# Optimization experiments

Measured on AMD Instinct MI355X. Metric: run time of the kernel, lower is better.

Reference implementation:

```python
import jax, jax.numpy as jnp
import numpy as np

CHUNK = 64   # hyperparams['chunk_size']
HEADS = 16   # hyperparams['n_heads']


def _chunk_mask(T, cs):
    # Faithful reproduction of the original (buggy) chunked mask:
    # for chunk pair with q-chunk start i and k-chunk start j, masking is applied
    # only when i >= j, with triu(diagonal = j - i + 1). Algebraically this masks
    # position (q, k) iff q_block_start >= k_block_start and
    #   (k - q) - 2*(k_block_start - q_block_start) >= 1.
    idx = jnp.arange(T)
    blk = (idx // cs) * cs  # chunk start of each position
    qb = blk[:, None]
    kb = blk[None, :]
    masked = (qb >= kb) & ((idx[None, :] - idx[:, None] - 2 * (kb - qb)) >= 1)
    return masked  # [T, T], True = set score to -inf


def setup_inputs() -> dict:
    key = jax.random.key(0)
    ks = jax.random.split(key, 6)
    B, T, C = 2, 2048, 1024
    w = 0.02  # init scale so softmax is not saturated
    return {
        "x": jax.random.normal(ks[0], (B, T, C), jnp.float32),
        "Wq": jax.random.normal(ks[1], (C, C), jnp.float32) * w,
        "bq": jnp.zeros((C,), jnp.float32),
        "Wk": jax.random.normal(ks[2], (C, C), jnp.float32) * w,
        "bk": jnp.zeros((C,), jnp.float32),
        "Wv": jax.random.normal(ks[3], (C, C), jnp.float32) * w,
        "bv": jnp.zeros((C,), jnp.float32),
        "Wo": jax.random.normal(ks[4], (C, C), jnp.float32) * w,
        "bo": jnp.zeros((C,), jnp.float32),
        "attn_scale": jnp.full((1,), 1.0 / np.sqrt(C // HEADS), jnp.float32),
    }


def reference(x, Wq, bq, Wk, bk, Wv, bv, Wo, bo, attn_scale):
    B, T, C = x.shape
    H = HEADS
    D = C // H
    # torch nn.Linear: y = x @ W.T + b
    q = (x @ Wq.T + bq).reshape(B, T, H, D)
    k = (x @ Wk.T + bk).reshape(B, T, H, D)
    v = (x @ Wv.T + bv).reshape(B, T, H, D)
    scores = jnp.einsum("bqhd,bkhd->bhqk", q, k) * attn_scale[0]
    mask = _chunk_mask(T, CHUNK)  # [T, T]
    scores = jnp.where(mask[None, None], -jnp.inf, scores)
    attn = jax.nn.softmax(scores, axis=-1)  # [B, H, T, T]
    out = jnp.einsum("bhqk,bkhd->bqhd", attn, v).reshape(B, T, C)
    return out @ Wo.T + bo
```

## Files before the change

### kernel.cpp

```cpp
#include <hip/hip_runtime.h>


#define BT 4096
#define TSEQ 2048
#define CDIM 1024

typedef __attribute__((ext_vector_type(8))) short bf16x8;
typedef __attribute__((ext_vector_type(4))) float f32x4;
typedef __attribute__((ext_vector_type(4))) float float4v;
typedef __attribute__((ext_vector_type(4))) unsigned short u16x4;

__device__ __forceinline__ unsigned short f2bf(float x){
  union { float f; unsigned int u; } c; c.f = x;
  unsigned int r = c.u + 0x7FFFu + ((c.u >> 16) & 1u);
  return (unsigned short)(r >> 16);
}
__device__ __forceinline__ float bf2f(unsigned short h){
  union { unsigned int u; float f; } c; c.u = ((unsigned int)h) << 16;
  return c.f;
}
__device__ __forceinline__ f32x4 zero4(){ f32x4 v; v[0]=0.f; v[1]=0.f; v[2]=0.f; v[3]=0.f; return v; }

#define GLDS16(g, l) __builtin_amdgcn_global_load_lds( \
  (const __attribute__((address_space(1))) void*)(g), \
  (__attribute__((address_space(3))) void*)(l), 16, 0, 0)

__global__ __launch_bounds__(256) void k_prep(
    const float* __restrict__ x,
    const float* __restrict__ Wq, const float* __restrict__ Wk,
    const float* __restrict__ Wv, const float* __restrict__ Wo,
    const float* __restrict__ bq, const float* __restrict__ bk, const float* __restrict__ bv,
    unsigned short* __restrict__ xh, unsigned short* __restrict__ wh,
    float* __restrict__ bias_cat){
  const int NX = 1048576;
  const int NTOT = 2097152;
  int i = blockIdx.x * 256 + threadIdx.x;
  if (i < 3072){
    const float* bs[3] = {bq, bk, bv};
    bias_cat[i] = bs[i >> 10][i & 1023];
  }
  int stride = gridDim.x * 256;
  for (; i < NTOT; i += stride){
    float4v v;
    u16x4 h;
    if (i < NX){
      v = ((const float4v*)x)[i];
      #pragma unroll
      for (int j = 0; j < 4; ++j) h[j] = f2bf(v[j]);
      ((u16x4*)xh)[i] = h;
    } else {
      int jj = i - NX;
      const float* srcs[4] = {Wq, Wk, Wv, Wo};
      v = ((const float4v*)srcs[jj >> 18])[jj & 0x3FFFF];
      #pragma unroll
      for (int j = 0; j < 4; ++j) h[j] = f2bf(v[j]);
      ((u16x4*)wh)[jj] = h;
    }
  }
}

template<int BN, int MODE, int SPLITA>
__global__ __launch_bounds__(256) void k_gemm(
    const unsigned short* __restrict__ Ah, const unsigned short* __restrict__ Al,
    const unsigned short* __restrict__ Bh,
    const float* __restrict__ bias,
    unsigned short* __restrict__ oq, unsigned short* __restrict__ okk,
    unsigned short* __restrict__ ov, float* __restrict__ fo)
{
  constexpr int MF = (BN == 128) ? 4 : 2;
  constexpr int NF = 4;
  constexpr int BISS = (BN == 128) ? 2 : 1;
  constexpr int NA = SPLITA ? 2 : 1;
  __shared__ unsigned short As[NA][128*32];
  __shared__ unsigned short Bs[BN*32];

  const int tid  = threadIdx.x;
  const int wid  = tid >> 6;
  const int lane = tid & 63;
  const int l15  = lane & 15;
  const int kg   = lane >> 4;
  const int m0 = blockIdx.y * 128;
  const int n0 = blockIdx.x * BN;
  const int wrb = (BN == 128) ? (wid >> 1) * 64 : wid * 32;
  const int wcb = (BN == 128) ? (wid & 1) * 64 : 0;

  f32x4 acc[MF][NF];
  #pragma unroll
  for (int a = 0; a < MF; ++a)
    #pragma unroll
    for (int b = 0; b < NF; ++b) acc[a][b] = zero4();

  for (int k0 = 0; k0 < 1024; k0 += 32){
    #pragma unroll
    for (int p = 0; p < NA; ++p){
      const unsigned short* Asrc = p ? Al : Ah;
      #pragma unroll
      for (int iss = 0; iss < 2; ++iss){
        int L = iss*2048 + tid*8;
        int row = L >> 5;
        int ck = ((L >> 3) & 3) ^ ((row >> 1) & 3);
        GLDS16(Asrc + (size_t)(m0 + row)*1024 + k0 + ck*8,
               (char*)(&As[p][0]) + iss*4096 + wid*1024);
      }
    }
    #pragma unroll
    for (int iss = 0; iss < BISS; ++iss){
      int L = iss*2048 + tid*8;
      int row = L >> 5;
      int ck = ((L >> 3) & 3) ^ ((row >> 1) & 3);
      GLDS16(Bh + (size_t)(n0 + row)*1024 + k0 + ck*8,
             (char*)(&Bs[0]) + iss*4096 + wid*1024);
    }
    __syncthreads();

    bf16x8 af[MF][NA];
    #pragma unroll
    for (int mf = 0; mf < MF; ++mf){
      int r = wrb + mf*16 + l15;
      int ckpos = kg ^ ((r >> 1) & 3);
      #pragma unroll
      for (int p = 0; p < NA; ++p)
        af[mf][p] = *(const bf16x8*)((const char*)(&As[p][0]) + r*64 + ckpos*16);
    }
    #pragma unroll
    for (int nf = 0; nf < NF; ++nf){
      int r = wcb + nf*16 + l15;
      int ckpos = kg ^ ((r >> 1) & 3);
      bf16x8 bhv = *(const bf16x8*)((const char*)(&Bs[0]) + r*64 + ckpos*16);
      #pragma unroll
      for (int mf = 0; mf < MF; ++mf){
        acc[mf][nf] = __builtin_amdgcn_mfma_f32_16x16x32_bf16(af[mf][0], bhv, acc[mf][nf], 0,0,0);
        if (SPLITA)
          acc[mf][nf] = __builtin_amdgcn_mfma_f32_16x16x32_bf16(af[mf][1], bhv, acc[mf][nf], 0,0,0);
      }
    }
    __syncthreads();
  }

  #pragma unroll
  for (int mf = 0; mf < MF; ++mf){
    #pragma unroll
    for (int nf = 0; nf < NF; ++nf){
      int colg = n0 + wcb + nf*16 + l15;
      float bb = bias[colg];
      #pragma unroll
      for (int j = 0; j < 4; ++j){
        int r = m0 + wrb + mf*16 + kg*4 + j;
        float val = acc[mf][nf][j] + bb;
        if (MODE == 1){
          fo[(size_t)r*1024 + colg] = val;
        } else {
          int bi = r >> 11, tt = r & 2047;
          int mat = colg >> 10, jj = colg & 1023;
          int h = jj >> 6, d = jj & 63;
          size_t bh_ = (size_t)(bi*16 + h);
          unsigned short vv = f2bf(val);
          if (mat == 0)      oq [(bh_*2048 + tt)*64 + d] = vv;
          else if (mat == 1) okk[(bh_*2048 + tt)*64 + d] = vv;
          else               ov [(bh_*64 + d)*2048 + tt] = vv;
        }
      }
    }
  }
}

__global__ __launch_bounds__(256) void k_attn(
    const unsigned short* __restrict__ Qg, const unsigned short* __restrict__ Kg,
    const unsigned short* __restrict__ Vtg, const float* __restrict__ scale_p,
    unsigned short* __restrict__ Ohi, unsigned short* __restrict__ Olo)
{
  __shared__ unsigned short Qs[64*64];
  __shared__ unsigned short Ks[64*64];
  __shared__ unsigned short Vts[64*64];
  __shared__ unsigned short Ps[4][16*64];

  const int tid  = threadIdx.x;
  const int wid  = tid >> 6;
  const int lane = tid & 63;
  const int l15  = lane & 15;
  const int kg   = lane >> 4;
  const int qi = blockIdx.x >> 5;
  const int bh = blockIdx.x & 31;
  const size_t base = (size_t)bh * (2048*64);
  const float scale = scale_p[0];

  #pragma unroll
  for (int iss = 0; iss < 2; ++iss){
    int L = iss*2048 + tid*8;
    int r = L >> 6;
    int ck = ((L >> 3) & 7) ^ (r & 7);
    GLDS16(Qg + base + (size_t)(qi*64 + r)*64 + ck*8, (char*)Qs + iss*4096 + wid*1024);
  }

  f32x4 Ofr[4];
  #pragma unroll
  for (int d = 0; d < 4; ++d) Ofr[d] = zero4();
  float mrow[4] = {-1e30f,-1e30f,-1e30f,-1e30f};
  float lrow[4] = {0.f,0.f,0.f,0.f};

  {
    int kb = qi;
    #pragma unroll
    for (int iss = 0; iss < 2; ++iss){
      int L = iss*2048 + tid*8;
      int r = L >> 6;
      int ck = ((L >> 3) & 7) ^ (r & 7);
      GLDS16(Kg  + base + (size_t)(kb*64 + r)*64 + ck*8, (char*)Ks  + iss*4096 + wid*1024);
      GLDS16(Vtg + base + (size_t)r*2048 + kb*64 + ck*8, (char*)Vts + iss*4096 + wid*1024);
    }
  }
  __syncthreads();

  for (int kb = qi; kb < 32; ++kb){
    f32x4 S[4];
    #pragma unroll
    for (int nf = 0; nf < 4; ++nf) S[nf] = zero4();
    #pragma unroll
    for (int ks = 0; ks < 2; ++ks){
      int rq = wid*16 + l15;
      bf16x8 aq = *(const bf16x8*)((const char*)Qs + rq*128 + (((ks*4 + kg) ^ (rq & 7)) * 16));
      #pragma unroll
      for (int nf = 0; nf < 4; ++nf){
        int rk = nf*16 + l15;
        bf16x8 bk_ = *(const bf16x8*)((const char*)Ks + rk*128 + (((ks*4 + kg) ^ (rk & 7)) * 16));
        S[nf] = __builtin_amdgcn_mfma_f32_16x16x32_bf16(aq, bk_, S[nf], 0,0,0);
      }
    }
    #pragma unroll
    for (int nf = 0; nf < 4; ++nf){
      #pragma unroll
      for (int j = 0; j < 4; ++j){
        float s = S[nf][j] * scale;
        if (kb == qi){
          int ql = wid*16 + kg*4 + j;
          int kk = nf*16 + l15;
          if (kk > ql) s = -1e30f;
        }
        S[nf][j] = s;
      }
    }
    float rm[4], fj[4], rs[4];
    #pragma unroll
    for (int j = 0; j < 4; ++j)
      rm[j] = fmaxf(fmaxf(S[0][j], S[1][j]), fmaxf(S[2][j], S[3][j]));
    #pragma unroll
    for (int d = 1; d < 16; d <<= 1){
      #pragma unroll
      for (int j = 0; j < 4; ++j) rm[j] = fmaxf(rm[j], __shfl_xor(rm[j], d, 64));
    }
    #pragma unroll
    for (int j = 0; j < 4; ++j){
      float mn = fmaxf(mrow[j], rm[j]);
      fj[j] = __expf(mrow[j] - mn);
      mrow[j] = mn;
      rs[j] = 0.f;
    }
    #pragma unroll
    for (int nf = 0; nf < 4; ++nf){
      #pragma unroll
      for (int j = 0; j < 4; ++j){
        float p = __expf(S[nf][j] - mrow[j]);
        S[nf][j] = p;
        rs[j] += p;
      }
    }
    #pragma unroll
    for (int d = 1; d < 16; d <<= 1){
      #pragma unroll
      for (int j = 0; j < 4; ++j) rs[j] += __shfl_xor(rs[j], d, 64);
    }
    #pragma unroll
    for (int j = 0; j < 4; ++j) lrow[j] = lrow[j]*fj[j] + rs[j];
    #pragma unroll
    for (int df = 0; df < 4; ++df){
      #pragma unroll
      for (int j = 0; j < 4; ++j) Ofr[df][j] *= fj[j];
    }
    #pragma unroll
    for (int nf = 0; nf < 4; ++nf){
      #pragma unroll
      for (int j = 0; j < 4; ++j){
        int r = kg*4 + j;
        int c2 = (nf*16 + l15) * 2;
        *(unsigned short*)((char*)(&Ps[wid][0]) + r*128 + (c2 ^ ((r & 7) << 4))) = f2bf(S[nf][j]);
      }
    }
    #pragma unroll
    for (int ks = 0; ks < 2; ++ks){
      bf16x8 pa = *(const bf16x8*)((const char*)(&Ps[wid][0]) + l15*128 + (((ks*4 + kg) ^ (l15 & 7)) * 16));
      #pragma unroll
      for (int df = 0; df < 4; ++df){
        int rv = df*16 + l15;
        bf16x8 vb = *(const bf16x8*)((const char*)Vts + rv*128 + (((ks*4 + kg) ^ (rv & 7)) * 16));
        Ofr[df] = __builtin_amdgcn_mfma_f32_16x16x32_bf16(pa, vb, Ofr[df], 0,0,0);
      }
    }
    __syncthreads();
    if (kb < 31){
      int kb2 = kb + 1;
      #pragma unroll
      for (int iss = 0; iss < 2; ++iss){
        int L = iss*2048 + tid*8;
        int r = L >> 6;
        int ck = ((L >> 3) & 7) ^ (r & 7);
        GLDS16(Kg  + base + (size_t)(kb2*64 + r)*64 + ck*8, (char*)Ks  + iss*4096 + wid*1024);
        GLDS16(Vtg + base + (size_t)r*2048 + kb2*64 + ck*8, (char*)Vts + iss*4096 + wid*1024);
      }
      __syncthreads();
    }
  }

  const int bi = bh >> 4, h = bh & 15;
  #pragma unroll
  for (int df = 0; df < 4; ++df){
    #pragma unroll
    for (int j = 0; j < 4; ++j){
      int tt = qi*64 + wid*16 + kg*4 + j;
      size_t row = (size_t)(bi*2048 + tt);
      int col = h*64 + df*16 + l15;
      float v = Ofr[df][j] / lrow[j];
      unsigned short hv = f2bf(v);
      Ohi[row*1024 + col] = hv;
      Olo[row*1024 + col] = f2bf(v - bf2f(hv));
    }
  }
}

extern "C" void kernel_launch(void* const* d_in, const int* in_sizes, int n_in,
                              void* d_out, int out_size, void* d_ws, size_t ws_size,
                              hipStream_t stream){
  const float* x  = (const float*)d_in[0];
  const float* Wq = (const float*)d_in[1];
  const float* bq = (const float*)d_in[2];
  const float* Wk = (const float*)d_in[3];
  const float* bk = (const float*)d_in[4];
  const float* Wv = (const float*)d_in[5];
  const float* bv = (const float*)d_in[6];
  const float* Wo = (const float*)d_in[7];
  const float* bo = (const float*)d_in[8];
  const float* scale = (const float*)d_in[9];
  float* out = (float*)d_out;

  char* ws = (char*)d_ws;
  const size_t MB = 1024*1024;
  unsigned short* xh  = (unsigned short*)(ws + 0*MB);
  unsigned short* wh  = (unsigned short*)(ws + 16*MB);
  unsigned short* Qb  = (unsigned short*)(ws + 32*MB);
  unsigned short* Kb  = (unsigned short*)(ws + 40*MB);
  unsigned short* Vtb = (unsigned short*)(ws + 48*MB);
  unsigned short* Ohi = (unsigned short*)(ws + 56*MB);
  unsigned short* Olo = (unsigned short*)(ws + 64*MB);
  float* bias_cat     = (float*)(ws + 72*MB);

  hipLaunchKernelGGL(k_prep, dim3(2048), dim3(256), 0, stream,
                     x, Wq, Wk, Wv, Wo, bq, bk, bv, xh, wh, bias_cat);
  hipLaunchKernelGGL((k_gemm<128,0,0>), dim3(24,32), dim3(256), 0, stream,
                     xh, (const unsigned short*)nullptr, wh, bias_cat,
                     Qb, Kb, Vtb, (float*)nullptr);
  hipLaunchKernelGGL(k_attn, dim3(1024), dim3(256), 0, stream, Qb, Kb, Vtb, scale, Ohi, Olo);
  hipLaunchKernelGGL((k_gemm<64,1,1>), dim3(16,32), dim3(256), 0, stream,
                     Ohi, Olo, wh + 3u*1048576u, bo,
                     (unsigned short*)nullptr, (unsigned short*)nullptr,
                     (unsigned short*)nullptr, out);
}
```

Before: 229.5 us.

## Double-buffer K/V in attention, transpose score layout, fold scale into Q projection

The attention kernel now double-buffers K and V tiles so the next block loads while the current one computes, and drops the extra barrier. It computes S transposed so each lane owns a single query row, which makes the row reductions cheaper. It also adds a lazy rescale that only updates the running max when it grows by more than a threshold, packs the bf16 conversions, and vectorises the output stores. The softmax scale moves into the Q projection epilogue, and the output projection switches to 128-wide tiles. The cost is more shared memory per block and lower precision margins in the softmax.

```diff
diff --git a/kernel.cpp b/kernel.cpp
--- a/kernel.cpp
+++ b/kernel.cpp
@@ -1,9 +1,5 @@
 #include <hip/hip_runtime.h>
 
-
-#define BT 4096
-#define TSEQ 2048
-#define CDIM 1024
 
 typedef __attribute__((ext_vector_type(8))) short bf16x8;
 typedef __attribute__((ext_vector_type(4))) float f32x4;
@@ -20,6 +16,11 @@
   return c.f;
 }
 __device__ __forceinline__ f32x4 zero4(){ f32x4 v; v[0]=0.f; v[1]=0.f; v[2]=0.f; v[3]=0.f; return v; }
+__device__ __forceinline__ unsigned int cvtpk(float a, float b){
+  unsigned int r;
+  asm("v_cvt_pk_bf16_f32 %0, %1, %2" : "=v"(r) : "v"(a), "v"(b));
+  return r;
+}
 
 #define GLDS16(g, l) __builtin_amdgcn_global_load_lds( \
   (const __attribute__((address_space(1))) void*)(g), \
@@ -63,7 +64,7 @@
 __global__ __launch_bounds__(256) void k_gemm(
     const unsigned short* __restrict__ Ah, const unsigned short* __restrict__ Al,
     const unsigned short* __restrict__ Bh,
-    const float* __restrict__ bias,
+    const float* __restrict__ bias, const float* __restrict__ scale_p,
     unsigned short* __restrict__ oq, unsigned short* __restrict__ okk,
     unsigned short* __restrict__ ov, float* __restrict__ fo)
 {
@@ -83,6 +84,7 @@
   const int n0 = blockIdx.x * BN;
   const int wrb = (BN == 128) ? (wid >> 1) * 64 : wid * 32;
   const int wcb = (BN == 128) ? (wid & 1) * 64 : 0;
+  const float qs = (MODE == 0) ? scale_p[0] : 0.f;
 
   f32x4 acc[MF][NF];
   #pragma unroll
@@ -154,10 +156,9 @@
           int mat = colg >> 10, jj = colg & 1023;
           int h = jj >> 6, d = jj & 63;
           size_t bh_ = (size_t)(bi*16 + h);
-          unsigned short vv = f2bf(val);
-          if (mat == 0)      oq [(bh_*2048 + tt)*64 + d] = vv;
-          else if (mat == 1) okk[(bh_*2048 + tt)*64 + d] = vv;
-          else               ov [(bh_*64 + d)*2048 + tt] = vv;
+          if (mat == 0)      oq [(bh_*2048 + tt)*64 + d] = f2bf(val * qs);
+          else if (mat == 1) okk[(bh_*2048 + tt)*64 + d] = f2bf(val);
+          else               ov [(bh_*64 + d)*2048 + tt] = f2bf(val);
         }
       }
     }
@@ -166,13 +167,13 @@
 
 __global__ __launch_bounds__(256) void k_attn(
     const unsigned short* __restrict__ Qg, const unsigned short* __restrict__ Kg,
-    const unsigned short* __restrict__ Vtg, const float* __restrict__ scale_p,
+    const unsigned short* __restrict__ Vtg,
     unsigned short* __restrict__ Ohi, unsigned short* __restrict__ Olo)
 {
   __shared__ unsigned short Qs[64*64];
-  __shared__ unsigned short Ks[64*64];
-  __shared__ unsigned short Vts[64*64];
-  __shared__ unsigned short Ps[4][16*64];
+  __shared__ unsigned short Ks[2][64*64];
+  __shared__ unsigned short Vts[2][64*64];
+  __shared__ unsigned short Pw[4][16*64];
 
   const int tid  = threadIdx.x;
   const int wid  = tid >> 6;
@@ -182,147 +183,133 @@
   const int qi = blockIdx.x >> 5;
   const int bh = blockIdx.x & 31;
   const size_t base = (size_t)bh * (2048*64);
-  const float scale = scale_p[0];
 
   #pragma unroll
   for (int iss = 0; iss < 2; ++iss){
     int L = iss*2048 + tid*8;
     int r = L >> 6;
     int ck = ((L >> 3) & 7) ^ (r & 7);
-    GLDS16(Qg + base + (size_t)(qi*64 + r)*64 + ck*8, (char*)Qs + iss*4096 + wid*1024);
-  }
-
-  f32x4 Ofr[4];
-  #pragma unroll
-  for (int d = 0; d < 4; ++d) Ofr[d] = zero4();
-  float mrow[4] = {-1e30f,-1e30f,-1e30f,-1e30f};
-  float lrow[4] = {0.f,0.f,0.f,0.f};
-
+    GLDS16(Qg  + base + (size_t)(qi*64 + r)*64 + ck*8, (char*)Qs + iss*4096 + wid*1024);
+    GLDS16(Kg  + base + (size_t)(qi*64 + r)*64 + ck*8, (char*)(&Ks[0][0])  + iss*4096 + wid*1024);
+    GLDS16(Vtg + base + (size_t)r*2048 + qi*64 + ck*8, (char*)(&Vts[0][0]) + iss*4096 + wid*1024);
+  }
+  __syncthreads();
+
+  bf16x8 qf[2];
   {
-    int kb = qi;
-    #pragma unroll
-    for (int iss = 0; iss < 2; ++iss){
-      int L = iss*2048 + tid*8;
-      int r = L >> 6;
-      int ck = ((L >> 3) & 7) ^ (r & 7);
-      GLDS16(Kg  + base + (size_t)(kb*64 + r)*64 + ck*8, (char*)Ks  + iss*4096 + wid*1024);
-      GLDS16(Vtg + base + (size_t)r*2048 + kb*64 + ck*8, (char*)Vts + iss*4096 + wid*1024);
-    }
-  }
-  __syncthreads();
+    int rq = wid*16 + l15;
+    #pragma unroll
+    for (int ks = 0; ks < 2; ++ks)
+      qf[ks] = *(const bf16x8*)((const char*)Qs + rq*128 + (((ks*4 + kg) ^ (rq & 7)) * 16));
+  }
+
+  f32x4 Ot[4];
+  #pragma unroll
+  for (int d = 0; d < 4; ++d) Ot[d] = zero4();
+  float m = -1e30f, l = 0.f;
+  const int qloc = wid*16 + l15;
+  char* pwb = (char*)(&Pw[wid][0]) + l15*128;
+  const int swz = (l15 & 7) << 4;
 
   for (int kb = qi; kb < 32; ++kb){
-    f32x4 S[4];
-    #pragma unroll
-    for (int nf = 0; nf < 4; ++nf) S[nf] = zero4();
-    #pragma unroll
-    for (int ks = 0; ks < 2; ++ks){
-      int rq = wid*16 + l15;
-      bf16x8 aq = *(const bf16x8*)((const char*)Qs + rq*128 + (((ks*4 + kg) ^ (rq & 7)) * 16));
-      #pragma unroll
-      for (int nf = 0; nf < 4; ++nf){
-        int rk = nf*16 + l15;
-        bf16x8 bk_ = *(const bf16x8*)((const char*)Ks + rk*128 + (((ks*4 + kg) ^ (rk & 7)) * 16));
-        S[nf] = __builtin_amdgcn_mfma_f32_16x16x32_bf16(aq, bk_, S[nf], 0,0,0);
-      }
-    }
-    #pragma unroll
-    for (int nf = 0; nf < 4; ++nf){
-      #pragma unroll
-      for (int j = 0; j < 4; ++j){
-        float s = S[nf][j] * scale;
-        if (kb == qi){
-          int ql = wid*16 + kg*4 + j;
-          int kk = nf*16 + l15;
-          if (kk > ql) s = -1e30f;
-        }
-        S[nf][j] = s;
-      }
-    }
-    float rm[4], fj[4], rs[4];
-    #pragma unroll
-    for (int j = 0; j < 4; ++j)
-      rm[j] = fmaxf(fmaxf(S[0][j], S[1][j]), fmaxf(S[2][j], S[3][j]));
-    #pragma unroll
-    for (int d = 1; d < 16; d <<= 1){
-      #pragma unroll
-      for (int j = 0; j < 4; ++j) rm[j] = fmaxf(rm[j], __shfl_xor(rm[j], d, 64));
-    }
-    #pragma unroll
-    for (int j = 0; j < 4; ++j){
-      float mn = fmaxf(mrow[j], rm[j]);
-      fj[j] = __expf(mrow[j] - mn);
-      mrow[j] = mn;
-      rs[j] = 0.f;
-    }
-    #pragma unroll
-    for (int nf = 0; nf < 4; ++nf){
-      #pragma unroll
-      for (int j = 0; j < 4; ++j){
-        float p = __expf(S[nf][j] - mrow[j]);
-        S[nf][j] = p;
-        rs[j] += p;
-      }
-    }
-    #pragma unroll
-    for (int d = 1; d < 16; d <<= 1){
-      #pragma unroll
-      for (int j = 0; j < 4; ++j) rs[j] += __shfl_xor(rs[j], d, 64);
-    }
-    #pragma unroll
-    for (int j = 0; j < 4; ++j) lrow[j] = lrow[j]*fj[j] + rs[j];
-    #pragma unroll
-    for (int df = 0; df < 4; ++df){
-      #pragma unroll
-      for (int j = 0; j < 4; ++j) Ofr[df][j] *= fj[j];
-    }
-    #pragma unroll
-    for (int nf = 0; nf < 4; ++nf){
-      #pragma unroll
-      for (int j = 0; j < 4; ++j){
-        int r = kg*4 + j;
-        int c2 = (nf*16 + l15) * 2;
-        *(unsigned short*)((char*)(&Ps[wid][0]) + r*128 + (c2 ^ ((r & 7) << 4))) = f2bf(S[nf][j]);
-      }
-    }
-    #pragma unroll
-    for (int ks = 0; ks < 2; ++ks){
-      bf16x8 pa = *(const bf16x8*)((const char*)(&Ps[wid][0]) + l15*128 + (((ks*4 + kg) ^ (l15 & 7)) * 16));
-      #pragma unroll
-      for (int df = 0; df < 4; ++df){
-        int rv = df*16 + l15;
-        bf16x8 vb = *(const bf16x8*)((const char*)Vts + rv*128 + (((ks*4 + kg) ^ (rv & 7)) * 16));
-        Ofr[df] = __builtin_amdgcn_mfma_f32_16x16x32_bf16(pa, vb, Ofr[df], 0,0,0);
-      }
-    }
-    __syncthreads();
-    if (kb < 31){
-      int kb2 = kb + 1;
+    const int buf = (kb - qi) & 1;
+    if (kb + 1 < 32){
+      int nb = buf ^ 1, kb2 = kb + 1;
       #pragma unroll
       for (int iss = 0; iss < 2; ++iss){
         int L = iss*2048 + tid*8;
         int r = L >> 6;
         int ck = ((L >> 3) & 7) ^ (r & 7);
-        GLDS16(Kg  + base + (size_t)(kb2*64 + r)*64 + ck*8, (char*)Ks  + iss*4096 + wid*1024);
-        GLDS16(Vtg + base + (size_t)r*2048 + kb2*64 + ck*8, (char*)Vts + iss*4096 + wid*1024);
-      }
-      __syncthreads();
-    }
+        GLDS16(Kg  + base + (size_t)(kb2*64 + r)*64 + ck*8, (char*)(&Ks[nb][0])  + iss*4096 + wid*1024);
+        GLDS16(Vtg + base + (size_t)r*2048 + kb2*64 + ck*8, (char*)(&Vts[nb][0]) + iss*4096 + wid*1024);
+      }
+    }
+    f32x4 ST[4];
+    #pragma unroll
+    for (int nf = 0; nf < 4; ++nf) ST[nf] = zero4();
+    #pragma unroll
+    for (int ks = 0; ks < 2; ++ks){
+      __builtin_amdgcn_s_setprio(1);
+      #pragma unroll
+      for (int nf = 0; nf < 4; ++nf){
+        int rk = nf*16 + l15;
+        bf16x8 ak = *(const bf16x8*)((const char*)(&Ks[buf][0]) + rk*128 + (((ks*4 + kg) ^ (rk & 7)) * 16));
+        ST[nf] = __builtin_amdgcn_mfma_f32_16x16x32_bf16(ak, qf[ks], ST[nf], 0,0,0);
+      }
+      __builtin_amdgcn_s_setprio(0);
+    }
+    if (kb == qi){
+      #pragma unroll
+      for (int nf = 0; nf < 4; ++nf)
+        #pragma unroll
+        for (int j = 0; j < 4; ++j)
+          if (nf*16 + kg*4 + j > qloc) ST[nf][j] = -1e30f;
+    }
+    float mx0 = fmaxf(fmaxf(ST[0][0], ST[0][1]), fmaxf(ST[0][2], ST[0][3]));
+    float mx1 = fmaxf(fmaxf(ST[1][0], ST[1][1]), fmaxf(ST[1][2], ST[1][3]));
+    float mx2 = fmaxf(fmaxf(ST[2][0], ST[2][1]), fmaxf(ST[2][2], ST[2][3]));
+    float mx3 = fmaxf(fmaxf(ST[3][0], ST[3][1]), fmaxf(ST[3][2], ST[3][3]));
+    float pmax = fmaxf(fmaxf(mx0, mx1), fmaxf(mx2, mx3));
+    pmax = fmaxf(pmax, __shfl_xor(pmax, 16, 64));
+    pmax = fmaxf(pmax, __shfl_xor(pmax, 32, 64));
+    if (!__all(pmax <= m + 8.0f)){
+      float mn = fmaxf(m, pmax);
+      float fj = __expf(m - mn);
+      m = mn;
+      l *= fj;
+      #pragma unroll
+      for (int df = 0; df < 4; ++df)
+        #pragma unroll
+        for (int j = 0; j < 4; ++j) Ot[df][j] *= fj;
+    }
+    float rsn[4];
+    unsigned int pk[4][2];
+    #pragma unroll
+    for (int nf = 0; nf < 4; ++nf){
+      float p0 = __expf(ST[nf][0] - m), p1 = __expf(ST[nf][1] - m);
+      float p2 = __expf(ST[nf][2] - m), p3 = __expf(ST[nf][3] - m);
+      rsn[nf] = (p0 + p1) + (p2 + p3);
+      pk[nf][0] = cvtpk(p0, p1);
+      pk[nf][1] = cvtpk(p2, p3);
+    }
+    float rs = (rsn[0] + rsn[1]) + (rsn[2] + rsn[3]);
+    rs += __shfl_xor(rs, 16, 64);
+    rs += __shfl_xor(rs, 32, 64);
+    l += rs;
+    #pragma unroll
+    for (int nf = 0; nf < 4; ++nf)
+      *(uint2*)(pwb + ((nf*32 + kg*8) ^ swz)) = make_uint2(pk[nf][0], pk[nf][1]);
+    #pragma unroll
+    for (int ks = 0; ks < 2; ++ks){
+      bf16x8 pa = *(const bf16x8*)(pwb + ((ks*64 + kg*16) ^ swz));
+      __builtin_amdgcn_s_setprio(1);
+      #pragma unroll
+      for (int df = 0; df < 4; ++df){
+        int rv = df*16 + l15;
+        bf16x8 vb = *(const bf16x8*)((const char*)(&Vts[buf][0]) + rv*128 + (((ks*4 + kg) ^ (rv & 7)) * 16));
+        Ot[df] = __builtin_amdgcn_mfma_f32_16x16x32_bf16(vb, pa, Ot[df], 0,0,0);
+      }
+      __builtin_amdgcn_s_setprio(0);
+    }
+    __syncthreads();
   }
 
   const int bi = bh >> 4, h = bh & 15;
+  const float rinv = 1.0f / l;
+  const size_t row = (size_t)(bi*2048 + qi*64 + qloc);
   #pragma unroll
   for (int df = 0; df < 4; ++df){
+    int colb = h*64 + df*16 + kg*4;
+    u16x4 hv, lv;
     #pragma unroll
     for (int j = 0; j < 4; ++j){
-      int tt = qi*64 + wid*16 + kg*4 + j;
-      size_t row = (size_t)(bi*2048 + tt);
-      int col = h*64 + df*16 + l15;
-      float v = Ofr[df][j] / lrow[j];
-      unsigned short hv = f2bf(v);
-      Ohi[row*1024 + col] = hv;
-      Olo[row*1024 + col] = f2bf(v - bf2f(hv));
-    }
+      float v = Ot[df][j] * rinv;
+      unsigned short hvv = f2bf(v);
+      hv[j] = hvv;
+      lv[j] = f2bf(v - bf2f(hvv));
+    }
+    *(u16x4*)(Ohi + row*1024 + colb) = hv;
+    *(u16x4*)(Olo + row*1024 + colb) = lv;
   }
 }
 
@@ -355,11 +342,11 @@
   hipLaunchKernelGGL(k_prep, dim3(2048), dim3(256), 0, stream,
                      x, Wq, Wk, Wv, Wo, bq, bk, bv, xh, wh, bias_cat);
   hipLaunchKernelGGL((k_gemm<128,0,0>), dim3(24,32), dim3(256), 0, stream,
-                     xh, (const unsigned short*)nullptr, wh, bias_cat,
+                     xh, (const unsigned short*)nullptr, wh, bias_cat, scale,
                      Qb, Kb, Vtb, (float*)nullptr);
-  hipLaunchKernelGGL(k_attn, dim3(1024), dim3(256), 0, stream, Qb, Kb, Vtb, scale, Ohi, Olo);
-  hipLaunchKernelGGL((k_gemm<64,1,1>), dim3(16,32), dim3(256), 0, stream,
-                     Ohi, Olo, wh + 3u*1048576u, bo,
+  hipLaunchKernelGGL(k_attn, dim3(1024), dim3(256), 0, stream, Qb, Kb, Vtb, Ohi, Olo);
+  hipLaunchKernelGGL((k_gemm<128,1,1>), dim3(8,32), dim3(256), 0, stream,
+                     Ohi, Olo, wh + 3u*1048576u, bo, (const float*)nullptr,
                      (unsigned short*)nullptr, (unsigned short*)nullptr,
                      (unsigned short*)nullptr, out);
 }
```

Measured after the change: 214.9 us. 1.07x faster.
